# Kernel optimization log

Measured on AMD Instinct MI355X. Metric: run time of the kernel, lower is better.

Reference implementation:

```python
import math
import jax, jax.numpy as jnp
import numpy as np

N_HEADS = 32
N_KV_HEADS = 8
HEAD_DIM = 64
DIM = 2048
BATCH = 1
SEQ = 2048


def setup_inputs() -> dict:
    key = jax.random.key(0)
    ks = jax.random.split(key, 7)
    x = jax.random.normal(ks[0], (BATCH, SEQ, DIM), dtype=jnp.float32)
    # RoPE frequencies, llama2.c style: [seq_len, head_dim//2]
    inv_freq = 1.0 / (10000.0 ** (np.arange(0, HEAD_DIM, 2, dtype=np.float32) / HEAD_DIM))
    t = np.arange(SEQ, dtype=np.float32)
    freqs = np.outer(t, inv_freq)  # [SEQ, HEAD_DIM//2]
    freqs_cos = jnp.asarray(np.cos(freqs), dtype=jnp.float32)
    freqs_sin = jnp.asarray(np.sin(freqs), dtype=jnp.float32)
    s = 0.02
    wq = jax.random.normal(ks[1], (N_HEADS * HEAD_DIM, DIM), dtype=jnp.float32) * s
    wk = jax.random.normal(ks[2], (N_KV_HEADS * HEAD_DIM, DIM), dtype=jnp.float32) * s
    wv = jax.random.normal(ks[3], (N_KV_HEADS * HEAD_DIM, DIM), dtype=jnp.float32) * s
    wo = jax.random.normal(ks[4], (DIM, N_HEADS * HEAD_DIM), dtype=jnp.float32) * s
    return {"x": x, "freqs_cos": freqs_cos, "freqs_sin": freqs_sin,
            "wq": wq, "wk": wk, "wv": wv, "wo": wo}


def _apply_rotary(q, k, cos, sin):
    # q: [B,S,H,D], k: [B,S,Hkv,D]; cos/sin: [S, D//2]
    def rot(t):
        tr = t[..., 0::2]  # real parts (even lanes)
        ti = t[..., 1::2]  # imag parts (odd lanes)
        c = cos[None, :, None, :]
        s = sin[None, :, None, :]
        out_r = tr * c - ti * s
        out_i = tr * s + ti * c
        # re-interleave
        return jnp.stack([out_r, out_i], axis=-1).reshape(t.shape)
    return rot(q), rot(k)


def reference(x, freqs_cos, freqs_sin, wq, wk, wv, wo):
    B, S, _ = x.shape
    n_rep = N_HEADS // N_KV_HEADS
    xq = (x @ wq.T).reshape(B, S, N_HEADS, HEAD_DIM)
    xk = (x @ wk.T).reshape(B, S, N_KV_HEADS, HEAD_DIM)
    xv = (x @ wv.T).reshape(B, S, N_KV_HEADS, HEAD_DIM)
    xq, xk = _apply_rotary(xq, xk, freqs_cos, freqs_sin)
    # repeat_kv: [B,S,Hkv,D] -> [B,S,Hkv*n_rep,D]
    xk = jnp.repeat(xk, n_rep, axis=2)
    xv = jnp.repeat(xv, n_rep, axis=2)
    # [B,H,S,D]
    q = xq.transpose(0, 2, 1, 3)
    k = xk.transpose(0, 2, 1, 3)
    v = xv.transpose(0, 2, 1, 3)
    scores = jnp.einsum('bhqd,bhkd->bhqk', q, k) / math.sqrt(HEAD_DIM)
    causal = jnp.triu(jnp.ones((S, S), dtype=bool), k=1)
    scores = jnp.where(causal[None, None], -jnp.inf, scores)
    weights = jax.nn.softmax(scores, axis=-1)
    out = jnp.einsum('bhqk,bhkd->bhqd', weights, v)
    out = out.transpose(0, 2, 1, 3).reshape(B, S, N_HEADS * HEAD_DIM)
    return out @ wo.T
```

## Files before the change

kernel.cpp:

```cpp
#include <hip/hip_runtime.h>
#include <hip/hip_bf16.h>

#define DIM 2048
#define SEQ 2048
#define HD 64
#define NH 32
#define NKV 8

typedef __bf16 bf16x8 __attribute__((ext_vector_type(8)));
typedef __bf16 bf16x4 __attribute__((ext_vector_type(4)));
typedef float f32x4 __attribute__((ext_vector_type(4)));
typedef float f32x16 __attribute__((ext_vector_type(16)));
typedef unsigned short ushortx8 __attribute__((ext_vector_type(8)));
typedef unsigned short ushortx4 __attribute__((ext_vector_type(4)));
typedef unsigned short ushort_t;

#define QSCALE 0.1803368801111f

__device__ __forceinline__ unsigned short f2bf(float f) {
    unsigned int u = __builtin_bit_cast(unsigned int, f);
    u = (u + 0x7FFFu + ((u >> 16) & 1u)) >> 16;
    return (unsigned short)u;
}

__device__ __forceinline__ f32x4 mfma16(bf16x8 a, bf16x8 b, f32x4 c) {
    return __builtin_amdgcn_mfma_f32_16x16x32_bf16(a, b, c, 0, 0, 0);
}
__device__ __forceinline__ f32x16 mfma32(bf16x8 a, bf16x8 b, f32x16 c) {
    return __builtin_amdgcn_mfma_f32_32x32x16_bf16(a, b, c, 0, 0, 0);
}

__device__ __forceinline__ void gload16(const ushort_t* g, ushort_t* l) {
    __builtin_amdgcn_global_load_lds(
        (const __attribute__((address_space(1))) unsigned int*)g,
        (__attribute__((address_space(3))) unsigned int*)l, 16, 0, 0);
}

#define NX  (SEQ * DIM)
#define NWQ (DIM * DIM)
#define NWK (NKV * HD * DIM)
#define NWO (DIM * NH * HD)

__global__ __launch_bounds__(256)
void cvt5(const float* __restrict__ x, const float* __restrict__ wq,
          const float* __restrict__ wk, const float* __restrict__ wv,
          const float* __restrict__ wo,
          ushort_t* __restrict__ xb, ushort_t* __restrict__ wqb,
          ushort_t* __restrict__ wkb, ushort_t* __restrict__ wvb,
          ushort_t* __restrict__ wob)
{
    const int S0 = NX / 4, S1 = S0 + NWQ / 4, S2 = S1 + NWK / 4,
              S3 = S2 + NWK / 4, S4 = S3 + NWO / 4;
    for (int g = blockIdx.x * blockDim.x + threadIdx.x; g < S4;
         g += gridDim.x * blockDim.x) {
        const float* src; ushort_t* dst; int off;
        if (g < S0)      { src = x;  dst = xb;  off = g; }
        else if (g < S1) { src = wq; dst = wqb; off = g - S0; }
        else if (g < S2) { src = wk; dst = wkb; off = g - S1; }
        else if (g < S3) { src = wv; dst = wvb; off = g - S2; }
        else             { src = wo; dst = wob; off = g - S3; }
        float4 v = ((const float4*)src)[off];
        ushortx4 h = { f2bf(v.x), f2bf(v.y), f2bf(v.z), f2bf(v.w) };
        ((ushortx4*)dst)[off] = h;
    }
}

__global__ __launch_bounds__(256)
void qkv_rope(const ushort_t* __restrict__ xb,
              const ushort_t* __restrict__ wqb, const ushort_t* __restrict__ wkb,
              const ushort_t* __restrict__ wvb,
              ushort_t* __restrict__ Qb, ushort_t* __restrict__ Kb,
              ushort_t* __restrict__ VtG,
              const float* __restrict__ cosp, const float* __restrict__ sinp)
{
    __shared__ ushort_t As[2][128 * 64];
    __shared__ ushort_t Bs[2][64 * 64];

    const int nt = blockIdx.x;
    const ushort_t* Bw; int bn0; int seg;
    if (nt < 32)      { seg = 0; Bw = wqb; bn0 = nt * 64; }
    else if (nt < 40) { seg = 1; Bw = wkb; bn0 = (nt - 32) * 64; }
    else              { seg = 2; Bw = wvb; bn0 = (nt - 40) * 64; }

    const int tid  = threadIdx.x;
    const int lane = tid & 63;
    const int wid  = tid >> 6;
    const int wr = wid >> 1, wc = wid & 1;
    const int bm0 = blockIdx.y * 128;
    const int g16 = lane >> 4, l16 = lane & 15;
    const int sr  = tid >> 3;
    const int scb = (tid & 7) * 16;
    const int scsw = (scb ^ ((sr & 7) << 4)) >> 1;
    const int xorb = (l16 & 7) << 4;

    f32x4 acc[4][2] = {};

    auto STAGE = [&](int k0, int b) {
#pragma unroll
        for (int i = 0; i < 4; i++) {
            int r = sr + i * 32;
            gload16(xb + (size_t)(bm0 + r) * DIM + k0 + scsw, &As[b][(i * 256 + tid) * 8]);
        }
#pragma unroll
        for (int i = 0; i < 2; i++) {
            int r = sr + i * 32;
            gload16(Bw + (size_t)(bn0 + r) * DIM + k0 + scsw, &Bs[b][(i * 256 + tid) * 8]);
        }
    };

    STAGE(0, 0);

    for (int k0 = 0; k0 < DIM; k0 += 64) {
        const int b = (k0 >> 6) & 1;
        __syncthreads();
        if (k0 + 64 < DIM) STAGE(k0 + 64, b ^ 1);
#pragma unroll
        for (int kk = 0; kk < 2; kk++) {
            const int ci = ((kk * 64 + g16 * 16) ^ xorb) >> 1;
            bf16x8 af[4], bfr[2];
#pragma unroll
            for (int mi = 0; mi < 4; mi++)
                af[mi] = *(const bf16x8*)&As[b][(wr * 64 + mi * 16 + l16) * 64 + ci];
#pragma unroll
            for (int ni = 0; ni < 2; ni++)
                bfr[ni] = *(const bf16x8*)&Bs[b][(wc * 32 + ni * 16 + l16) * 64 + ci];
#pragma unroll
            for (int mi = 0; mi < 4; mi++)
#pragma unroll
                for (int ni = 0; ni < 2; ni++)
                    acc[mi][ni] = mfma16(af[mi], bfr[ni], acc[mi][ni]);
        }
    }

#pragma unroll
    for (int mi = 0; mi < 4; mi++) {
#pragma unroll
        for (int ni = 0; ni < 2; ni++) {
            const int row0 = bm0 + wr * 64 + mi * 16 + g16 * 4;
            const int col  = bn0 + wc * 32 + ni * 16 + l16;
            f32x4 v = acc[mi][ni];
            if (seg <= 1) {
                ushort_t* C = (seg == 0) ? Qb : Kb;
                const int ldC = (seg == 0) ? NH * HD : NKV * HD;
                const int d   = col & (HD - 1);
                const int p   = d >> 1;
                const bool odd = d & 1;
#pragma unroll
                for (int r = 0; r < 4; r++) {
                    float val = v[r];
                    float partner = __shfl_xor(val, 1);
                    int m = row0 + r;
                    float c = cosp[m * (HD / 2) + p];
                    float s = sinp[m * (HD / 2) + p];
                    float o = odd ? (partner * s + val * c) : (val * c - partner * s);
                    if (seg == 0) o *= QSCALE;
                    C[(size_t)m * ldC + col] = f2bf(o);
                }
            } else {
                const int pg = ((g16 & 1) << 1) | (g16 >> 1);
                const int rowp = bm0 + wr * 64 + mi * 16 + pg * 4;
                ushortx4 hv = { f2bf(v[0]), f2bf(v[1]), f2bf(v[2]), f2bf(v[3]) };
                *(ushortx4*)&VtG[(size_t)col * SEQ + rowp] = hv;
            }
        }
    }
}

__global__ __launch_bounds__(128)
void attn_fwd(const ushort_t* __restrict__ Q,
              const ushort_t* __restrict__ K,
              const ushort_t* __restrict__ VtG,
              ushort_t* __restrict__ O)
{
    __shared__ ushort_t Ks[2][64 * 64];
    __shared__ ushort_t Vt[2][64 * 64];

    const int h  = blockIdx.x;
    const int qi = 31 - blockIdx.y;
    const int kh = h >> 2;
    const int tid = threadIdx.x;
    const int lane = tid & 63;
    const int w = tid >> 6;
    const int l32 = lane & 31;
    const int hi  = lane >> 5;
    const int sr = tid >> 3;
    const int scb = (tid & 7) * 16;
    const int scsw = (scb ^ ((sr & 7) << 4)) >> 1;
    const int rx = (l32 & 7) << 4;

    const int qw = qi * 64 + w * 32;
    const int nkt = qi + 1;

    bf16x8 qf[4];
#pragma unroll
    for (int ds = 0; ds < 4; ds++)
        qf[ds] = *(const bf16x8*)&Q[(size_t)(qw + l32) * (NH * HD) + h * HD + ds * 16 + hi * 8];

    f32x16 accO0 = {}, accO1 = {};
    float lsum = 0.f;

    auto STAGE = [&](int kt, int bf) {
#pragma unroll
        for (int i = 0; i < 4; i++) {
            int row = sr + i * 16;
            gload16(K   + (size_t)(kt * 64 + row) * (NKV * HD) + kh * HD + scsw,
                    &Ks[bf][(i * 128 + tid) * 8]);
            gload16(VtG + (size_t)(kh * HD + row) * SEQ + kt * 64 + scsw,
                    &Vt[bf][(i * 128 + tid) * 8]);
        }
    };

    STAGE(0, 0);

    for (int kj = 0; kj < nkt; kj++) {
        const int b = kj & 1;
        const int kb = kj * 64;
        __syncthreads();
        if (kj + 1 < nkt) STAGE(kj + 1, b ^ 1);

        if (kb <= qw + 31) {
            f32x16 s0 = {}, s1 = {};
            __builtin_amdgcn_s_setprio(1);
#pragma unroll
            for (int ds = 0; ds < 4; ds++) {
                const int ci = (((32 * ds + 16 * hi)) ^ rx) >> 1;
                bf16x8 kf0 = *(const bf16x8*)&Ks[b][(l32)      * 64 + ci];
                bf16x8 kf1 = *(const bf16x8*)&Ks[b][(32 + l32) * 64 + ci];
                s0 = mfma32(kf0, qf[ds], s0);
                s1 = mfma32(kf1, qf[ds], s1);
            }
            __builtin_amdgcn_s_setprio(0);

            if (kb + 63 > qw) {
                const int qg = qw + l32;
#pragma unroll
                for (int r = 0; r < 16; r++) {
                    const int kl = (r & 3) + 8 * (r >> 2) + 4 * hi;
                    if (kb + kl > qg)      s0[r] = -1e30f;
                    if (kb + 32 + kl > qg) s1[r] = -1e30f;
                }
            }

            float p0[16], p1[16];
#pragma unroll
            for (int r = 0; r < 16; r++) { p0[r] = exp2f(s0[r]); p1[r] = exp2f(s1[r]); }
#pragma unroll
            for (int r = 0; r < 16; r++) lsum += p0[r] + p1[r];
            bf16x8 pa00, pa01, pa10, pa11;
#pragma unroll
            for (int e = 0; e < 8; e++) {
                pa00[e] = (__bf16)p0[e];  pa01[e] = (__bf16)p0[8 + e];
                pa10[e] = (__bf16)p1[e];  pa11[e] = (__bf16)p1[8 + e];
            }

            __builtin_amdgcn_s_setprio(1);
#pragma unroll
            for (int s = 0; s < 4; s++) {
                bf16x8 pa = (s == 0) ? pa00 : (s == 1) ? pa01 : (s == 2) ? pa10 : pa11;
                const int ci = (((32 * s + 16 * hi)) ^ rx) >> 1;
                bf16x8 vf0 = *(const bf16x8*)&Vt[b][(l32)      * 64 + ci];
                bf16x8 vf1 = *(const bf16x8*)&Vt[b][(32 + l32) * 64 + ci];
                accO0 = mfma32(pa, vf0, accO0);
                accO1 = mfma32(pa, vf1, accO1);
            }
            __builtin_amdgcn_s_setprio(0);
        }
    }

    lsum += __shfl_xor(lsum, 32);

#pragma unroll
    for (int r = 0; r < 16; r++) {
        const int qr = (r & 3) + 8 * (r >> 2) + 4 * hi;
        float ls = __shfl(lsum, qr);
        float inv = 1.0f / ls;
        size_t base = (size_t)(qw + qr) * (NH * HD) + h * HD;
        O[base + l32]      = f2bf(accO0[r] * inv);
        O[base + 32 + l32] = f2bf(accO1[r] * inv);
    }
}

__global__ __launch_bounds__(256)
void gemm_out(const ushort_t* __restrict__ A, const ushort_t* __restrict__ Bw,
              float* __restrict__ C)
{
    __shared__ ushort_t As[2][128 * 64];
    __shared__ ushort_t Bs[2][64 * 64];

    const int tid  = threadIdx.x;
    const int lane = tid & 63;
    const int wid  = tid >> 6;
    const int wr = wid >> 1, wc = wid & 1;
    const int bm0 = blockIdx.y * 128, bn0 = blockIdx.x * 64;
    const int g16 = lane >> 4, l16 = lane & 15;
    const int sr  = tid >> 3;
    const int scb = (tid & 7) * 16;
    const int scsw = (scb ^ ((sr & 7) << 4)) >> 1;
    const int xorb = (l16 & 7) << 4;

    f32x4 acc[4][2] = {};

    auto STAGE = [&](int k0, int b) {
#pragma unroll
        for (int i = 0; i < 4; i++) {
            int r = sr + i * 32;
            gload16(A + (size_t)(bm0 + r) * DIM + k0 + scsw, &As[b][(i * 256 + tid) * 8]);
        }
#pragma unroll
        for (int i = 0; i < 2; i++) {
            int r = sr + i * 32;
            gload16(Bw + (size_t)(bn0 + r) * DIM + k0 + scsw, &Bs[b][(i * 256 + tid) * 8]);
        }
    };

    STAGE(0, 0);

    for (int k0 = 0; k0 < DIM; k0 += 64) {
        const int b = (k0 >> 6) & 1;
        __syncthreads();
        if (k0 + 64 < DIM) STAGE(k0 + 64, b ^ 1);
#pragma unroll
        for (int kk = 0; kk < 2; kk++) {
            const int ci = ((kk * 64 + g16 * 16) ^ xorb) >> 1;
            bf16x8 af[4], bfr[2];
#pragma unroll
            for (int mi = 0; mi < 4; mi++)
                af[mi] = *(const bf16x8*)&As[b][(wr * 64 + mi * 16 + l16) * 64 + ci];
#pragma unroll
            for (int ni = 0; ni < 2; ni++)
                bfr[ni] = *(const bf16x8*)&Bs[b][(wc * 32 + ni * 16 + l16) * 64 + ci];
#pragma unroll
            for (int mi = 0; mi < 4; mi++)
#pragma unroll
                for (int ni = 0; ni < 2; ni++)
                    acc[mi][ni] = mfma16(af[mi], bfr[ni], acc[mi][ni]);
        }
    }

#pragma unroll
    for (int mi = 0; mi < 4; mi++) {
#pragma unroll
        for (int ni = 0; ni < 2; ni++) {
            const int row0 = bm0 + wr * 64 + mi * 16 + g16 * 4;
            const int col  = bn0 + wc * 32 + ni * 16 + l16;
#pragma unroll
            for (int r = 0; r < 4; r++)
                C[(size_t)(row0 + r) * DIM + col] = acc[mi][ni][r];
        }
    }
}

extern "C" void kernel_launch(void* const* d_in, const int* in_sizes, int n_in,
                              void* d_out, int out_size, void* d_ws, size_t ws_size,
                              hipStream_t stream)
{
    (void)in_sizes; (void)n_in; (void)out_size; (void)ws_size;
    const float* x    = (const float*)d_in[0];
    const float* fcos = (const float*)d_in[1];
    const float* fsin = (const float*)d_in[2];
    const float* wq   = (const float*)d_in[3];
    const float* wk   = (const float*)d_in[4];
    const float* wv   = (const float*)d_in[5];
    const float* wo   = (const float*)d_in[6];
    float* out = (float*)d_out;

    char* ws = (char*)d_ws;
    size_t off = 0;
    ushort_t* xb  = (ushort_t*)(ws + off); off += (size_t)NX  * 2;
    ushort_t* wqb = (ushort_t*)(ws + off); off += (size_t)NWQ * 2;
    ushort_t* wkb = (ushort_t*)(ws + off); off += (size_t)NWK * 2;
    ushort_t* wvb = (ushort_t*)(ws + off); off += (size_t)NWK * 2;
    ushort_t* wob = (ushort_t*)(ws + off); off += (size_t)NWO * 2;
    ushort_t* Qb  = (ushort_t*)(ws + off); off += (size_t)SEQ * NH * HD * 2;
    ushort_t* Kb  = (ushort_t*)(ws + off); off += (size_t)SEQ * NKV * HD * 2;
    ushort_t* VtG = (ushort_t*)(ws + off); off += (size_t)SEQ * NKV * HD * 2;
    ushort_t* Ab  = (ushort_t*)(ws + off);

    dim3 blk(256);
    cvt5<<<dim3(2048), blk, 0, stream>>>(x, wq, wk, wv, wo, xb, wqb, wkb, wvb, wob);
    qkv_rope<<<dim3(48, 16), blk, 0, stream>>>(xb, wqb, wkb, wvb, Qb, Kb, VtG, fcos, fsin);
    attn_fwd<<<dim3(32, 32), dim3(128), 0, stream>>>(Qb, Kb, VtG, Ab);
    gemm_out<<<dim3(32, 16), blk, 0, stream>>>(Ab, wob, out);
}
```

Before: 144.7 us.

## Split causal attention into KV chunks with separate reduction kernel

Attention blocks now cover 128 query rows with 256 threads and process a chunk of at most 8 KV tiles, so the long causal rows are split across several blocks and the work per block is more even. Each block writes unnormalized fp32 partial outputs and row sums to a workspace, and a new reduce kernel sums the chunks, normalizes and converts to bf16. The split only works because the softmax apparently uses a fixed max (no running max), so partials can be added directly. It adds a kernel launch and extra fp32 traffic for the partial outputs.

```diff
diff --git a/kernel.cpp b/kernel.cpp
--- a/kernel.cpp
+++ b/kernel.cpp
@@ -16,6 +16,9 @@
 typedef unsigned short ushort_t;
 
 #define QSCALE 0.1803368801111f
+
+#define CHUNK 8
+#define SLOTS_PER_H 40
 
 __device__ __forceinline__ unsigned short f2bf(float f) {
     unsigned int u = __builtin_bit_cast(unsigned int, f);
@@ -166,18 +169,28 @@
     }
 }
 
-__global__ __launch_bounds__(128)
+__global__ __launch_bounds__(256)
 void attn_fwd(const ushort_t* __restrict__ Q,
               const ushort_t* __restrict__ K,
               const ushort_t* __restrict__ VtG,
-              ushort_t* __restrict__ O)
+              float* __restrict__ Opart, float* __restrict__ Lpart)
 {
     __shared__ ushort_t Ks[2][64 * 64];
     __shared__ ushort_t Vt[2][64 * 64];
 
     const int h  = blockIdx.x;
-    const int qi = 31 - blockIdx.y;
     const int kh = h >> 2;
+    int y = blockIdx.y, qi = 0, pref = 0;
+    for (;;) {
+        int nch = (2 * qi + 9) >> 3;
+        if (y < nch) break;
+        y -= nch; pref += nch; qi++;
+    }
+    const int c = y;
+    const int kt0 = c * CHUNK;
+    const int ktN = min(kt0 + CHUNK, 2 * qi + 2);
+    const int sidx = h * SLOTS_PER_H + pref + c;
+
     const int tid = threadIdx.x;
     const int lane = tid & 63;
     const int w = tid >> 6;
@@ -188,8 +201,7 @@
     const int scsw = (scb ^ ((sr & 7) << 4)) >> 1;
     const int rx = (l32 & 7) << 4;
 
-    const int qw = qi * 64 + w * 32;
-    const int nkt = qi + 1;
+    const int qw = qi * 128 + w * 32;
 
     bf16x8 qf[4];
 #pragma unroll
@@ -201,22 +213,22 @@
 
     auto STAGE = [&](int kt, int bf) {
 #pragma unroll
-        for (int i = 0; i < 4; i++) {
-            int row = sr + i * 16;
+        for (int i = 0; i < 2; i++) {
+            int row = sr + i * 32;
             gload16(K   + (size_t)(kt * 64 + row) * (NKV * HD) + kh * HD + scsw,
-                    &Ks[bf][(i * 128 + tid) * 8]);
+                    &Ks[bf][(i * 256 + tid) * 8]);
             gload16(VtG + (size_t)(kh * HD + row) * SEQ + kt * 64 + scsw,
-                    &Vt[bf][(i * 128 + tid) * 8]);
+                    &Vt[bf][(i * 256 + tid) * 8]);
         }
     };
 
-    STAGE(0, 0);
-
-    for (int kj = 0; kj < nkt; kj++) {
-        const int b = kj & 1;
+    STAGE(kt0, 0);
+
+    for (int kj = kt0; kj < ktN; kj++) {
+        const int b = (kj - kt0) & 1;
         const int kb = kj * 64;
         __syncthreads();
-        if (kj + 1 < nkt) STAGE(kj + 1, b ^ 1);
+        if (kj + 1 < ktN) STAGE(kj + 1, b ^ 1);
 
         if (kb <= qw + 31) {
             f32x16 s0 = {}, s1 = {};
@@ -269,15 +281,46 @@
 
     lsum += __shfl_xor(lsum, 32);
 
+    float* op = Opart + (size_t)sidx * (128 * 64);
 #pragma unroll
     for (int r = 0; r < 16; r++) {
         const int qr = (r & 3) + 8 * (r >> 2) + 4 * hi;
-        float ls = __shfl(lsum, qr);
-        float inv = 1.0f / ls;
-        size_t base = (size_t)(qw + qr) * (NH * HD) + h * HD;
-        O[base + l32]      = f2bf(accO0[r] * inv);
-        O[base + 32 + l32] = f2bf(accO1[r] * inv);
-    }
+        float* rowp = op + (size_t)(w * 32 + qr) * 64;
+        rowp[l32]      = accO0[r];
+        rowp[32 + l32] = accO1[r];
+    }
+    if (hi == 0) Lpart[sidx * 128 + w * 32 + l32] = lsum;
+}
+
+__global__ __launch_bounds__(256)
+void attn_reduce(const float* __restrict__ Opart, const float* __restrict__ Lpart,
+                 ushort_t* __restrict__ Ab)
+{
+    const int gid = blockIdx.x * 256 + threadIdx.x;
+    const int g = gid & 7;
+    const int h = (gid >> 3) & 31;
+    const int m = gid >> 8;
+    const int qi = m >> 7, rr = m & 127;
+    int pref = 0;
+#pragma unroll
+    for (int q = 0; q < 16; q++) pref += (q < qi) ? ((2 * q + 9) >> 3) : 0;
+    const int nch = (2 * qi + 9) >> 3;
+    const int sbase = h * SLOTS_PER_H + pref;
+
+    f32x4 sa = {}, sb = {};
+    float l = 0.f;
+    for (int c = 0; c < nch; c++) {
+        const float* rowp = Opart + ((size_t)(sbase + c) * 128 + rr) * 64 + g * 8;
+        f32x4 a = *(const f32x4*)rowp;
+        f32x4 b = *(const f32x4*)(rowp + 4);
+        sa += a; sb += b;
+        l += Lpart[(sbase + c) * 128 + rr];
+    }
+    const float inv = 1.0f / l;
+    ushortx8 o;
+#pragma unroll
+    for (int e = 0; e < 4; e++) { o[e] = f2bf(sa[e] * inv); o[4 + e] = f2bf(sb[e] * inv); }
+    *(ushortx8*)&Ab[(size_t)m * (NH * HD) + h * 64 + g * 8] = o;
 }
 
 __global__ __launch_bounds__(256)
@@ -374,11 +417,14 @@
     ushort_t* Qb  = (ushort_t*)(ws + off); off += (size_t)SEQ * NH * HD * 2;
     ushort_t* Kb  = (ushort_t*)(ws + off); off += (size_t)SEQ * NKV * HD * 2;
     ushort_t* VtG = (ushort_t*)(ws + off); off += (size_t)SEQ * NKV * HD * 2;
-    ushort_t* Ab  = (ushort_t*)(ws + off);
+    ushort_t* Ab  = (ushort_t*)(ws + off); off += (size_t)SEQ * NH * HD * 2;
+    float* Opart  = (float*)(ws + off);    off += (size_t)32 * SLOTS_PER_H * 128 * 64 * 4;
+    float* Lpart  = (float*)(ws + off);    off += (size_t)32 * SLOTS_PER_H * 128 * 4;
 
     dim3 blk(256);
     cvt5<<<dim3(2048), blk, 0, stream>>>(x, wq, wk, wv, wo, xb, wqb, wkb, wvb, wob);
     qkv_rope<<<dim3(48, 16), blk, 0, stream>>>(xb, wqb, wkb, wvb, Qb, Kb, VtG, fcos, fsin);
-    attn_fwd<<<dim3(32, 32), dim3(128), 0, stream>>>(Qb, Kb, VtG, Ab);
+    attn_fwd<<<dim3(32, SLOTS_PER_H), blk, 0, stream>>>(Qb, Kb, VtG, Opart, Lpart);
+    attn_reduce<<<dim3(2048), blk, 0, stream>>>(Opart, Lpart, Ab);
     gemm_out<<<dim3(32, 16), blk, 0, stream>>>(Ab, wob, out);
 }
```

Result: faster. 136.0 us (-6.0%).
